# Performance work log

Measured on AMD Instinct MI355X. Metric: run time of the kernel, lower is better.

Reference implementation:

```python
import jax, jax.numpy as jnp
import numpy as np

BETA = 0.25  # commitment loss coefficient


def setup_inputs() -> dict:
    key = jax.random.key(0)
    kx, kc = jax.random.split(key)
    # x: [B, T, D] latents; codebooks: [M, K, D] (equal K per level -> stacked)
    x = jax.random.normal(kx, (64, 1024, 256), dtype=jnp.float32)
    # small init akin to RandomUniform(-1/K, 1/K)
    codebooks = jax.random.normal(kc, (4, 1024, 256), dtype=jnp.float32) * (1.0 / 1024.0)
    return {"x": x, "codebooks": codebooks}


def reference(x, codebooks):
    """Residual VQ forward (inference path: no EMA state update).

    Returns (y, commit_loss): y = x + stop_grad(sum_l q_l - x) (straight-through),
    commit_loss = beta * sum_l mean((stop_grad(q_l) - r_l)^2).
    """
    D = x.shape[-1]
    M = codebooks.shape[0]
    flat = x.reshape(-1, D)                      # [N, D]
    residual = flat
    q_sum = jnp.zeros_like(flat)
    commit = jnp.zeros((), dtype=x.dtype)
    for lvl in range(M):                         # M is small & fixed (4)
        cb = codebooks[lvl]                      # [K, D]
        # squared L2 distances: ||r||^2 + ||e||^2 - 2 r.e^T
        r2 = jnp.sum(residual * residual, axis=1, keepdims=True)   # [N, 1]
        e2 = jnp.sum(cb * cb, axis=1)                               # [K]
        dist = r2 + e2 - 2.0 * jnp.matmul(residual, cb.T)           # [N, K]
        idx = jnp.argmin(dist, axis=1)                              # [N]
        q = jnp.take(cb, idx, axis=0)                               # [N, D]
        q_st = jax.lax.stop_gradient(q)
        commit = commit + BETA * jnp.mean((q_st - residual) ** 2)
        q_sum = q_sum + q
        residual = residual - q_st
    y_flat = flat + jax.lax.stop_gradient(q_sum - flat)
    return y_flat.reshape(x.shape), commit
```

## Files before the change

### kernel.cpp

```cpp
#include <hip/hip_runtime.h>

#define DIM 256
#define KCODES 1024
#define LEVELS 4
#define CHUNK 64
#define NCHUNK 16
#define TOKB 128
#define NTOK 65536
#define NELEM (NTOK * DIM)

typedef _Float16 h8 __attribute__((ext_vector_type(8)));
typedef _Float16 h4 __attribute__((ext_vector_type(4)));
typedef _Float16 h2 __attribute__((ext_vector_type(2)));
typedef float f4 __attribute__((ext_vector_type(4)));
typedef float fx16 __attribute__((ext_vector_type(16)));
typedef unsigned int u32;

__device__ __forceinline__ void gload16(const void* g, void* l) {
  __builtin_amdgcn_global_load_lds(
      (const __attribute__((address_space(1))) void*)g,
      (__attribute__((address_space(3))) void*)l, 16, 0, 0);
}

__device__ __forceinline__ float sq8(h8 r, float acc) {
#if __has_builtin(__builtin_amdgcn_fdot2)
  #pragma unroll
  for (int j = 0; j < 4; ++j) {
    h2 p = {r[2 * j], r[2 * j + 1]};
    acc = __builtin_amdgcn_fdot2(p, p, acc, false);
  }
#else
  #pragma unroll
  for (int j = 0; j < 8; ++j) { float v = (float)r[j]; acc += v * v; }
#endif
  return acc;
}

__global__ __launch_bounds__(256) void rvq_prep(const float* __restrict__ cb,
                                                _Float16* __restrict__ cb16,
                                                float* __restrict__ e2p,
                                                float* __restrict__ out) {
  if (blockIdx.x == 0 && threadIdx.x == 0) out[NELEM] = 0.0f;
  const int row = blockIdx.x * 4 + (threadIdx.x >> 6);
  const int lane = threadIdx.x & 63;
  const float* src = cb + (size_t)row * DIM + lane * 4;
  f4 v = *(const f4*)src;
  h4 hv;
  hv[0] = (_Float16)v[0]; hv[1] = (_Float16)v[1];
  hv[2] = (_Float16)v[2]; hv[3] = (_Float16)v[3];
  *(h4*)(cb16 + (size_t)row * DIM + lane * 4) = hv;
  float s = v[0]*v[0] + v[1]*v[1] + v[2]*v[2] + v[3]*v[3];
  #pragma unroll
  for (int off = 32; off; off >>= 1) s += __shfl_xor(s, off, 64);
  if (lane == 0) e2p[row] = 0.25f - 0.5f * s;
}

__global__ __launch_bounds__(128, 1) void rvq_main(
    const float* __restrict__ x, const float* __restrict__ cb32,
    const _Float16* __restrict__ cb16, const float* __restrict__ e2p,
    float* __restrict__ out) {
  __shared__ __attribute__((aligned(16))) _Float16 clds[2][CHUNK * DIM];
  __shared__ __attribute__((aligned(16))) float e2_lds[KCODES];
  __shared__ __attribute__((aligned(16))) int idx_hist[TOKB][4];
  __shared__ float r2_sh[TOKB];
  __shared__ float csum_sh[2];

  const int tid = threadIdx.x;
  const int wave = tid >> 6, lane = tid & 63;
  const int Llo = lane & 31, Lhi = lane >> 5;

  int s4[4], rd4[4];
  #pragma unroll
  for (int j = 0; j < 4; ++j) {
    const int key = (2 * j + Lhi) & 7;
    s4[j] = (wave * 32 + 2 * j + Lhi) * 512 + ((Llo ^ key) << 4);
    rd4[j] = (key ^ (Llo & 7)) << 4;
  }

  const char* cb16b = (const char*)cb16;
  {
    char* ldst = (char*)&clds[0][0] + wave * 16384;
    #pragma unroll
    for (int i = 0; i < 16; ++i)
      gload16(cb16b + s4[i & 3] + (i >> 2) * 4096, ldst + i * 1024);
  }

  h8 af[2][16];
  float r2p[2] = {0.f, 0.f};
  const size_t tok0 = (size_t)blockIdx.x * TOKB + wave * 64;
  #pragma unroll
  for (int mt = 0; mt < 2; ++mt) {
    const float* xr = x + (tok0 + mt * 32 + Llo) * DIM + Lhi * 8;
    #pragma unroll
    for (int kk = 0; kk < 16; ++kk) {
      f4 a = *(const f4*)(xr + kk * 16);
      f4 b = *(const f4*)(xr + kk * 16 + 4);
      h8 h;
      #pragma unroll
      for (int j = 0; j < 4; ++j) { h[j] = (_Float16)a[j]; h[4 + j] = (_Float16)b[j]; }
      af[mt][kk] = h;
      r2p[mt] = sq8(h, r2p[mt]);
    }
  }

  float commit_acc = 0.f;

  for (int lvl = 0; lvl < LEVELS; ++lvl) {
    #pragma unroll
    for (int mt = 0; mt < 2; ++mt) {
      float s = r2p[mt] + __shfl_xor(r2p[mt], 32, 64);
      if (Lhi == 0) r2_sh[wave * 64 + mt * 32 + Llo] = s;
    }
    *(f4*)&e2_lds[tid * 8] = *(const f4*)(e2p + (lvl << 10) + tid * 8);
    *(f4*)&e2_lds[tid * 8 + 4] = *(const f4*)(e2p + (lvl << 10) + tid * 8 + 4);

    u32 best[2][16];
    #pragma unroll
    for (int mt = 0; mt < 2; ++mt)
      #pragma unroll
      for (int i = 0; i < 16; ++i) best[mt][i] = 0u;

    for (int c = 0; c < NCHUNK; ++c) {
      __syncthreads();
      {
        const int gn = lvl * NCHUNK + c + 1;
        const char* gsrc = cb16b + ((size_t)(gn < 64 ? gn : 63) << 15);
        char* ldst = (char*)&clds[(c + 1) & 1][0] + wave * 16384;
        #pragma unroll
        for (int i = 0; i < 16; ++i)
          gload16(gsrc + s4[i & 3] + (i >> 2) * 4096, ldst + i * 1024);
      }

      const char* cbuf = (const char*)&clds[c & 1][0];
      #pragma unroll
      for (int nt = 0; nt < 2; ++nt) {
        const int code0 = c * 64 + nt * 32;
        const float e2v = e2_lds[code0 + Llo];
        fx16 acc0, acc1;
        #pragma unroll
        for (int i = 0; i < 16; ++i) { acc0[i] = e2v; acc1[i] = e2v; }
        const char* bptr = cbuf + (nt * 32 + Llo) * 512;
        #pragma unroll
        for (int kk = 0; kk < 16; ++kk) {
          h8 b = *(const h8*)(bptr + rd4[kk & 3] + (kk >> 2) * 128);
          acc0 = __builtin_amdgcn_mfma_f32_32x32x16_f16(af[0][kk], b, acc0, 0, 0, 0);
          acc1 = __builtin_amdgcn_mfma_f32_32x32x16_f16(af[1][kk], b, acc1, 0, 0, 0);
        }
        const u32 invc = ((u32)(code0 + Llo)) ^ 1023u;
        #pragma unroll
        for (int i = 0; i < 16; ++i) {
          u32 p0 = (__float_as_uint(acc0[i]) & 0xFFFFFC00u) | invc;
          if (p0 > best[0][i]) best[0][i] = p0;
          u32 p1 = (__float_as_uint(acc1[i]) & 0xFFFFFC00u) | invc;
          if (p1 > best[1][i]) best[1][i] = p1;
        }
      }
    }

    #pragma unroll
    for (int mt = 0; mt < 2; ++mt)
      #pragma unroll
      for (int i = 0; i < 16; ++i) {
        u32 b = best[mt][i];
        #pragma unroll
        for (int off = 1; off < 32; off <<= 1) {
          u32 o = __shfl_xor(b, off, 32);
          if (o > b) b = o;
        }
        best[mt][i] = b;
      }

    if (Llo == 0) {
      #pragma unroll
      for (int mt = 0; mt < 2; ++mt)
        #pragma unroll
        for (int i = 0; i < 16; ++i) {
          const u32 p = best[mt][i];
          const int code = (int)((p & 1023u) ^ 1023u);
          const int t = wave * 64 + mt * 32 + (i & 3) + 8 * (i >> 2) + 4 * Lhi;
          idx_hist[t][lvl] = code;
          const float sc = __uint_as_float(p & 0xFFFFFC00u) - 0.25f;
          commit_acc += r2_sh[t] - 2.0f * sc;
        }
    }
    __syncthreads();

    if (lvl < LEVELS - 1) {
      r2p[0] = 0.f; r2p[1] = 0.f;
      #pragma unroll
      for (int mt = 0; mt < 2; ++mt) {
        const int qidx = idx_hist[wave * 64 + mt * 32 + Llo][lvl];
        const _Float16* qr = cb16 + (((size_t)lvl << 10) + qidx) * DIM + Lhi * 8;
        #pragma unroll
        for (int kk = 0; kk < 16; ++kk) {
          h8 q = *(const h8*)(qr + kk * 16);
          h8 r = af[mt][kk] - q;
          af[mt][kk] = r;
          r2p[mt] = sq8(r, r2p[mt]);
        }
      }
    }
  }

  float* yblk = out + (size_t)blockIdx.x * (TOKB * DIM);
  #pragma unroll 4
  for (int it = 0; it < 64; ++it) {
    const int f = it * 512 + tid * 4;
    const int t = f >> 8;
    const int d = f & 255;
    const int4 qi = *(const int4*)&idx_hist[t][0];
    f4 q0 = *(const f4*)(cb32 + (size_t)qi.x * DIM + d);
    f4 q1 = *(const f4*)(cb32 + (size_t)(1024 + qi.y) * DIM + d);
    f4 q2 = *(const f4*)(cb32 + (size_t)(2048 + qi.z) * DIM + d);
    f4 q3 = *(const f4*)(cb32 + (size_t)(3072 + qi.w) * DIM + d);
    f4 yv = (q0 + q1) + (q2 + q3);
    *(f4*)(yblk + f) = yv;
  }

  #pragma unroll
  for (int off = 1; off < 64; off <<= 1) commit_acc += __shfl_xor(commit_acc, off, 64);
  if (lane == 0) csum_sh[wave] = commit_acc;
  __syncthreads();
  if (tid == 0) {
    atomicAdd(out + NELEM, (csum_sh[0] + csum_sh[1]) * (0.25f / 16777216.0f));
  }
}

extern "C" void kernel_launch(void* const* d_in, const int* in_sizes, int n_in,
                              void* d_out, int out_size, void* d_ws, size_t ws_size,
                              hipStream_t stream) {
  const float* x = (const float*)d_in[0];
  const float* cb = (const float*)d_in[1];
  float* out = (float*)d_out;
  _Float16* cb16 = (_Float16*)d_ws;
  float* e2p = (float*)((char*)d_ws + (size_t)LEVELS * KCODES * DIM * sizeof(_Float16));

  rvq_prep<<<(LEVELS * KCODES) / 4, 256, 0, stream>>>(cb, cb16, e2p, out);
  rvq_main<<<NTOK / TOKB, 128, 0, stream>>>(x, cb, cb16, e2p, out);
}
```

Before: 293.4 us.

## Split block into four waves of 32 tokens each with new LDS codebook layout

Each 128-token block now runs 256 threads (four waves) instead of two, so each wave owns 32 tokens and keeps half as many A-fragment and best-index registers. Launch bounds now request two blocks per CU. The codebook chunk LDS layout moves from an XOR-swizzled row layout to a k-major fragment layout, so each lane reads its B fragment at lane*16 bytes without a swizzle. The aim is more waves in flight to hide latency, at the cost of each B fragment feeding one MFMA instead of two, which doubles LDS reads per MFMA.

```diff
diff --git a/kernel.cpp b/kernel.cpp
--- a/kernel.cpp
+++ b/kernel.cpp
@@ -55,7 +55,7 @@
   if (lane == 0) e2p[row] = 0.25f - 0.5f * s;
 }
 
-__global__ __launch_bounds__(128, 1) void rvq_main(
+__global__ __launch_bounds__(256, 2) void rvq_main(
     const float* __restrict__ x, const float* __restrict__ cb32,
     const _Float16* __restrict__ cb16, const float* __restrict__ e2p,
     float* __restrict__ out) {
@@ -63,34 +63,29 @@
   __shared__ __attribute__((aligned(16))) float e2_lds[KCODES];
   __shared__ __attribute__((aligned(16))) int idx_hist[TOKB][4];
   __shared__ float r2_sh[TOKB];
-  __shared__ float csum_sh[2];
+  __shared__ float csum_sh[4];
 
   const int tid = threadIdx.x;
   const int wave = tid >> 6, lane = tid & 63;
   const int Llo = lane & 31, Lhi = lane >> 5;
 
-  int s4[4], rd4[4];
-  #pragma unroll
-  for (int j = 0; j < 4; ++j) {
-    const int key = (2 * j + Lhi) & 7;
-    s4[j] = (wave * 32 + 2 * j + Lhi) * 512 + ((Llo ^ key) << 4);
-    rd4[j] = (key ^ (Llo & 7)) << 4;
-  }
-
+  const int snt = wave >> 1, sk0 = (wave & 1) << 3;
+  const int sg_off = (snt * 32 + Llo) * 512 + (sk0 << 5) + (Lhi << 4);
+  const int sl_off = (snt * 16 + sk0) << 10;
   const char* cb16b = (const char*)cb16;
+
   {
-    char* ldst = (char*)&clds[0][0] + wave * 16384;
-    #pragma unroll
-    for (int i = 0; i < 16; ++i)
-      gload16(cb16b + s4[i & 3] + (i >> 2) * 4096, ldst + i * 1024);
-  }
-
-  h8 af[2][16];
-  float r2p[2] = {0.f, 0.f};
-  const size_t tok0 = (size_t)blockIdx.x * TOKB + wave * 64;
-  #pragma unroll
-  for (int mt = 0; mt < 2; ++mt) {
-    const float* xr = x + (tok0 + mt * 32 + Llo) * DIM + Lhi * 8;
+    const char* gsrc = cb16b + sg_off;
+    char* ldst = (char*)&clds[0][0] + sl_off;
+    #pragma unroll
+    for (int i = 0; i < 8; ++i) gload16(gsrc + i * 32, ldst + i * 1024);
+  }
+
+  h8 af[16];
+  float r2p = 0.f;
+  const size_t tok0 = (size_t)blockIdx.x * TOKB + wave * 32;
+  {
+    const float* xr = x + (tok0 + Llo) * DIM + Lhi * 8;
     #pragma unroll
     for (int kk = 0; kk < 16; ++kk) {
       f4 a = *(const f4*)(xr + kk * 16);
@@ -98,114 +93,100 @@
       h8 h;
       #pragma unroll
       for (int j = 0; j < 4; ++j) { h[j] = (_Float16)a[j]; h[4 + j] = (_Float16)b[j]; }
-      af[mt][kk] = h;
-      r2p[mt] = sq8(h, r2p[mt]);
+      af[kk] = h;
+      r2p = sq8(h, r2p);
     }
   }
 
   float commit_acc = 0.f;
 
   for (int lvl = 0; lvl < LEVELS; ++lvl) {
-    #pragma unroll
-    for (int mt = 0; mt < 2; ++mt) {
-      float s = r2p[mt] + __shfl_xor(r2p[mt], 32, 64);
-      if (Lhi == 0) r2_sh[wave * 64 + mt * 32 + Llo] = s;
-    }
-    *(f4*)&e2_lds[tid * 8] = *(const f4*)(e2p + (lvl << 10) + tid * 8);
-    *(f4*)&e2_lds[tid * 8 + 4] = *(const f4*)(e2p + (lvl << 10) + tid * 8 + 4);
-
-    u32 best[2][16];
-    #pragma unroll
-    for (int mt = 0; mt < 2; ++mt)
-      #pragma unroll
-      for (int i = 0; i < 16; ++i) best[mt][i] = 0u;
+    {
+      float s = r2p + __shfl_xor(r2p, 32, 64);
+      if (Lhi == 0) r2_sh[wave * 32 + Llo] = s;
+    }
+    *(f4*)&e2_lds[tid * 4] = *(const f4*)(e2p + (lvl << 10) + tid * 4);
+
+    u32 best[16];
+    #pragma unroll
+    for (int i = 0; i < 16; ++i) best[i] = 0u;
 
     for (int c = 0; c < NCHUNK; ++c) {
       __syncthreads();
       {
         const int gn = lvl * NCHUNK + c + 1;
-        const char* gsrc = cb16b + ((size_t)(gn < 64 ? gn : 63) << 15);
-        char* ldst = (char*)&clds[(c + 1) & 1][0] + wave * 16384;
+        const char* gsrc = cb16b + ((size_t)(gn < 64 ? gn : 63) << 15) + sg_off;
+        char* ldst = (char*)&clds[(c + 1) & 1][0] + sl_off;
         #pragma unroll
-        for (int i = 0; i < 16; ++i)
-          gload16(gsrc + s4[i & 3] + (i >> 2) * 4096, ldst + i * 1024);
-      }
-
-      const char* cbuf = (const char*)&clds[c & 1][0];
-      #pragma unroll
-      for (int nt = 0; nt < 2; ++nt) {
-        const int code0 = c * 64 + nt * 32;
-        const float e2v = e2_lds[code0 + Llo];
-        fx16 acc0, acc1;
-        #pragma unroll
-        for (int i = 0; i < 16; ++i) { acc0[i] = e2v; acc1[i] = e2v; }
-        const char* bptr = cbuf + (nt * 32 + Llo) * 512;
-        #pragma unroll
-        for (int kk = 0; kk < 16; ++kk) {
-          h8 b = *(const h8*)(bptr + rd4[kk & 3] + (kk >> 2) * 128);
-          acc0 = __builtin_amdgcn_mfma_f32_32x32x16_f16(af[0][kk], b, acc0, 0, 0, 0);
-          acc1 = __builtin_amdgcn_mfma_f32_32x32x16_f16(af[1][kk], b, acc1, 0, 0, 0);
-        }
-        const u32 invc = ((u32)(code0 + Llo)) ^ 1023u;
-        #pragma unroll
-        for (int i = 0; i < 16; ++i) {
-          u32 p0 = (__float_as_uint(acc0[i]) & 0xFFFFFC00u) | invc;
-          if (p0 > best[0][i]) best[0][i] = p0;
-          u32 p1 = (__float_as_uint(acc1[i]) & 0xFFFFFC00u) | invc;
-          if (p1 > best[1][i]) best[1][i] = p1;
-        }
-      }
-    }
-
-    #pragma unroll
-    for (int mt = 0; mt < 2; ++mt)
+        for (int i = 0; i < 8; ++i) gload16(gsrc + i * 32, ldst + i * 1024);
+      }
+
+      const char* cbuf = (const char*)&clds[c & 1][0] + (lane << 4);
+      const float e0 = e2_lds[c * 64 + Llo];
+      const float e1 = e2_lds[c * 64 + 32 + Llo];
+      fx16 acc0, acc1;
+      #pragma unroll
+      for (int i = 0; i < 16; ++i) { acc0[i] = e0; acc1[i] = e1; }
+      #pragma unroll
+      for (int kk = 0; kk < 16; ++kk) {
+        h8 b0 = *(const h8*)(cbuf + (kk << 10));
+        h8 b1 = *(const h8*)(cbuf + ((16 + kk) << 10));
+        acc0 = __builtin_amdgcn_mfma_f32_32x32x16_f16(af[kk], b0, acc0, 0, 0, 0);
+        acc1 = __builtin_amdgcn_mfma_f32_32x32x16_f16(af[kk], b1, acc1, 0, 0, 0);
+      }
+      const u32 invc0 = ((u32)(c * 64 + Llo)) ^ 1023u;
+      const u32 invc1 = ((u32)(c * 64 + 32 + Llo)) ^ 1023u;
       #pragma unroll
       for (int i = 0; i < 16; ++i) {
-        u32 b = best[mt][i];
-        #pragma unroll
-        for (int off = 1; off < 32; off <<= 1) {
-          u32 o = __shfl_xor(b, off, 32);
-          if (o > b) b = o;
-        }
-        best[mt][i] = b;
-      }
+        u32 p0 = (__float_as_uint(acc0[i]) & 0xFFFFFC00u) | invc0;
+        if (p0 > best[i]) best[i] = p0;
+        u32 p1 = (__float_as_uint(acc1[i]) & 0xFFFFFC00u) | invc1;
+        if (p1 > best[i]) best[i] = p1;
+      }
+    }
+
+    #pragma unroll
+    for (int i = 0; i < 16; ++i) {
+      u32 b = best[i];
+      #pragma unroll
+      for (int off = 1; off < 32; off <<= 1) {
+        u32 o = __shfl_xor(b, off, 32);
+        if (o > b) b = o;
+      }
+      best[i] = b;
+    }
 
     if (Llo == 0) {
       #pragma unroll
-      for (int mt = 0; mt < 2; ++mt)
-        #pragma unroll
-        for (int i = 0; i < 16; ++i) {
-          const u32 p = best[mt][i];
-          const int code = (int)((p & 1023u) ^ 1023u);
-          const int t = wave * 64 + mt * 32 + (i & 3) + 8 * (i >> 2) + 4 * Lhi;
-          idx_hist[t][lvl] = code;
-          const float sc = __uint_as_float(p & 0xFFFFFC00u) - 0.25f;
-          commit_acc += r2_sh[t] - 2.0f * sc;
-        }
+      for (int i = 0; i < 16; ++i) {
+        const u32 p = best[i];
+        const int code = (int)((p & 1023u) ^ 1023u);
+        const int t = wave * 32 + (i & 3) + 8 * (i >> 2) + 4 * Lhi;
+        idx_hist[t][lvl] = code;
+        const float sc = __uint_as_float(p & 0xFFFFFC00u) - 0.25f;
+        commit_acc += r2_sh[t] - 2.0f * sc;
+      }
     }
     __syncthreads();
 
     if (lvl < LEVELS - 1) {
-      r2p[0] = 0.f; r2p[1] = 0.f;
-      #pragma unroll
-      for (int mt = 0; mt < 2; ++mt) {
-        const int qidx = idx_hist[wave * 64 + mt * 32 + Llo][lvl];
-        const _Float16* qr = cb16 + (((size_t)lvl << 10) + qidx) * DIM + Lhi * 8;
-        #pragma unroll
-        for (int kk = 0; kk < 16; ++kk) {
-          h8 q = *(const h8*)(qr + kk * 16);
-          h8 r = af[mt][kk] - q;
-          af[mt][kk] = r;
-          r2p[mt] = sq8(r, r2p[mt]);
-        }
+      r2p = 0.f;
+      const int qidx = idx_hist[wave * 32 + Llo][lvl];
+      const _Float16* qr = cb16 + (((size_t)lvl << 10) + qidx) * DIM + Lhi * 8;
+      #pragma unroll
+      for (int kk = 0; kk < 16; ++kk) {
+        h8 q = *(const h8*)(qr + kk * 16);
+        h8 r = af[kk] - q;
+        af[kk] = r;
+        r2p = sq8(r, r2p);
       }
     }
   }
 
   float* yblk = out + (size_t)blockIdx.x * (TOKB * DIM);
   #pragma unroll 4
-  for (int it = 0; it < 64; ++it) {
-    const int f = it * 512 + tid * 4;
+  for (int it = 0; it < 32; ++it) {
+    const int f = it * 1024 + tid * 4;
     const int t = f >> 8;
     const int d = f & 255;
     const int4 qi = *(const int4*)&idx_hist[t][0];
@@ -222,7 +203,8 @@
   if (lane == 0) csum_sh[wave] = commit_acc;
   __syncthreads();
   if (tid == 0) {
-    atomicAdd(out + NELEM, (csum_sh[0] + csum_sh[1]) * (0.25f / 16777216.0f));
+    const float tot = csum_sh[0] + csum_sh[1] + csum_sh[2] + csum_sh[3];
+    atomicAdd(out + NELEM, tot * (0.25f / 16777216.0f));
   }
 }
 
@@ -236,5 +218,5 @@
   float* e2p = (float*)((char*)d_ws + (size_t)LEVELS * KCODES * DIM * sizeof(_Float16));
 
   rvq_prep<<<(LEVELS * KCODES) / 4, 256, 0, stream>>>(cb, cb16, e2p, out);
-  rvq_main<<<NTOK / TOKB, 128, 0, stream>>>(x, cb, cb16, e2p, out);
-}
+  rvq_main<<<NTOK / TOKB, 256, 0, stream>>>(x, cb, cb16, e2p, out);
+}
```

After: 278.1 us. 5.2% less time.
